# Optimization experiments

Hardware: AMD Instinct MI355X
Metric: run time of the kernel (lower is better)

Reference implementation:

```python
import jax, jax.numpy as jnp
import numpy as np

B = 4194304  # batch
H = 32       # hidden width of TinyMLP


def _xavier(key, fan_in, fan_out, gain=0.5):
    lim = gain * np.sqrt(6.0 / (fan_in + fan_out))
    return jax.random.uniform(key, (fan_in, fan_out), jnp.float32, -lim, lim)


def setup_inputs() -> dict:
    key = jax.random.key(0)
    ks = jax.random.split(key, 7)
    return {
        "x1": jax.random.normal(ks[0], (B,), jnp.float32),
        "x2": jax.random.normal(ks[1], (B,), jnp.float32),
        "y1": jax.random.normal(ks[2], (B,), jnp.float32),
        "y2": jax.random.normal(ks[3], (B,), jnp.float32),
        "W1": _xavier(ks[4], 2, H),
        "b1": jnp.zeros((H,), jnp.float32),
        "W2": _xavier(ks[5], H, H),
        "b2": jnp.zeros((H,), jnp.float32),
        "W3": _xavier(ks[6], H, 1),
        "b3": jnp.zeros((1,), jnp.float32),
    }


def reference(x1, x2, y1, y2, W1, b1, W2, b2, W3, b3):
    # Y: [B, 2]
    Y = jnp.stack([y1, y2], axis=1)

    def F_sum(Yv):
        h1 = jax.nn.sigmoid(Yv @ W1 + b1)   # [B, H]
        h2 = jax.nn.sigmoid(h1 @ W2 + b2)   # [B, H]
        return jnp.sum(h2 @ W3 + b3)        # scalar sum of F values

    dF_dY = jax.grad(F_sum)(Y)              # [B, 2], analytic input-gradient

    x1_out = x1 + dF_dY[:, 0]
    x2_out = x2 + dF_dY[:, 1]
    # Stack the 4 output streams as columns: (x1', x2', y1, y2)
    return jnp.stack([x1_out, x2_out, y1, y2], axis=1)
```

## Files before the change

### kernel.cpp

```cpp
#include <hip/hip_runtime.h>


#define H 32

typedef __attribute__((ext_vector_type(8))) short bf16x8;
typedef __attribute__((ext_vector_type(4))) float f32x4;
typedef __attribute__((ext_vector_type(2))) float f32x2;
typedef __attribute__((ext_vector_type(2))) __bf16 bfx2;

__device__ __forceinline__ int cvt_pk_bf16(float a, float b) {
    f32x2 f; f[0] = a; f[1] = b;
    bfx2 r = __builtin_convertvector(f, bfx2);
    return __builtin_bit_cast(int, r);
}

__device__ __forceinline__ unsigned short f2bf_trunc(float f) {
    unsigned u = __builtin_bit_cast(unsigned, f);
    return (unsigned short)((u + 0x8000u) >> 16);
}

#define NLOG2E (-1.4426950408889634f)

__global__ __launch_bounds__(256) void tinymlp_mfma_kernel(
    const float* __restrict__ x1, const float* __restrict__ x2,
    const float* __restrict__ y1, const float* __restrict__ y2,
    const float* __restrict__ W1, const float* __restrict__ b1,
    const float* __restrict__ W2, const float* __restrict__ b2,
    const float* __restrict__ W3,
    float4* __restrict__ out, int ntiles)
{
    __shared__ unsigned short lds_dz2[4][512];
    __shared__ float          lds_dh1[4][512];

    const int tid  = threadIdx.x;
    const int w    = tid >> 6;
    const int lane = tid & 63;
    const int m    = lane & 15;
    const int q    = lane >> 4;
    const int kb   = q * 8;

    bf16x8 bW2s_0, bW2s_1, bW2T_0, bW2T_1, bW1r;
    float w1a[8], w1b[8], b1v[8];
    #pragma unroll
    for (int j = 0; j < 8; ++j) {
        bW2s_0[j] = (short)f2bf_trunc(NLOG2E * W2[(kb + j) * H + m]);
        bW2s_1[j] = (short)f2bf_trunc(NLOG2E * W2[(kb + j) * H + m + 16]);
        bW2T_0[j] = (short)f2bf_trunc(W2[m * H + kb + j]);
        bW2T_1[j] = (short)f2bf_trunc(W2[(m + 16) * H + kb + j]);
        bW1r[j]   = (short)f2bf_trunc(W1[(m & 1) * H + kb + j]);
        w1a[j] = NLOG2E * W1[kb + j];
        w1b[j] = NLOG2E * W1[H + kb + j];
        b1v[j] = NLOG2E * b1[kb + j];
    }
    const float b2s0 = NLOG2E * b2[m];
    const float b2s1 = NLOG2E * b2[m + 16];
    f32x2 w3v; w3v[0] = W3[m]; w3v[1] = W3[m + 16];

    const int gwave  = (blockIdx.x * blockDim.x + tid) >> 6;
    const int nwaves = (gridDim.x * blockDim.x) >> 6;

    const int c    = m & 3;
    const int srow = q * 4 + c;
    const long start = (long)gwave * 16;
    const long step  = (long)nwaves * 16;
    const float* py1 = y1 + start + m;
    const float* py2 = y2 + start + m;
    const float* px1 = x1 + start + srow;
    const float* px2 = x2 + start + srow;
    const float* qy1 = y1 + start + srow;
    const float* qy2 = y2 + start + srow;
    float4*      po  = out + start + srow;

    unsigned short* dzp = &lds_dz2[w][(m >> 3) * 128 + (m & 7) + q * 32];

    for (int tile = gwave; tile < ntiles; tile += nwaves) {
        const float y1v = *py1;
        const float y2v = *py2;
        float xv1 = 0.f, xv2 = 0.f, yv3 = 0.f, yv4 = 0.f;
        if (m < 4) { xv1 = *px1; xv2 = *px2; yv3 = *qy1; yv4 = *qy2; }

        f32x2 h1dp[4];
        union { int i[4]; bf16x8 v; } uaH;
        #pragma unroll
        for (int t = 0; t < 4; ++t) {
            const int j = 2 * t;
            float z0 = fmaf(y1v, w1a[j],     fmaf(y2v, w1b[j],     b1v[j]));
            float z1 = fmaf(y1v, w1a[j + 1], fmaf(y2v, w1b[j + 1], b1v[j + 1]));
            float e0 = __builtin_amdgcn_exp2f(z0);
            float e1 = __builtin_amdgcn_exp2f(z1);
            float s0 = __builtin_amdgcn_rcpf(1.0f + e0);
            float s1 = __builtin_amdgcn_rcpf(1.0f + e1);
            f32x2 sv; sv[0] = s0; sv[1] = s1;
            h1dp[t] = __builtin_elementwise_fma(-sv, sv, sv);
            uaH.i[t] = cvt_pk_bf16(s0, s1);
        }

        f32x4 accZ0 = {b2s0, b2s0, b2s0, b2s0};
        f32x4 accZ1 = {b2s1, b2s1, b2s1, b2s1};
        accZ0 = __builtin_amdgcn_mfma_f32_16x16x32_bf16(uaH.v, bW2s_0, accZ0, 0, 0, 0);
        accZ1 = __builtin_amdgcn_mfma_f32_16x16x32_bf16(uaH.v, bW2s_1, accZ1, 0, 0, 0);

        #pragma unroll
        for (int r = 0; r < 4; ++r) {
            float e0 = __builtin_amdgcn_exp2f(accZ0[r]);
            float e1 = __builtin_amdgcn_exp2f(accZ1[r]);
            float s0 = __builtin_amdgcn_rcpf(1.0f + e0);
            float s1 = __builtin_amdgcn_rcpf(1.0f + e1);
            f32x2 sv; sv[0] = s0; sv[1] = s1;
            f32x2 dv = __builtin_elementwise_fma(-sv, sv, sv) * w3v;
            unsigned pk = (unsigned)cvt_pk_bf16(dv[0], dv[1]);
            dzp[r * 8]       = (unsigned short)pk;
            dzp[r * 8 + 256] = (unsigned short)(pk >> 16);
        }
        __builtin_amdgcn_wave_barrier();

        const bf16x8 aD = *(const bf16x8*)&lds_dz2[w][lane * 8];
        f32x4 accD0 = {0.f, 0.f, 0.f, 0.f}, accD1 = {0.f, 0.f, 0.f, 0.f};
        accD0 = __builtin_amdgcn_mfma_f32_16x16x32_bf16(aD, bW2T_0, accD0, 0, 0, 0);
        accD1 = __builtin_amdgcn_mfma_f32_16x16x32_bf16(aD, bW2T_1, accD1, 0, 0, 0);

        #pragma unroll
        for (int r = 0; r < 4; ++r) {
            const int row = q * 4 + r;
            lds_dh1[w][row * 32 + (((m >> 3) ^ r) << 3) + (m & 7)]       = accD0[r];
            lds_dh1[w][row * 32 + ((((m >> 3) | 2) ^ r) << 3) + (m & 7)] = accD1[r];
        }
        __builtin_amdgcn_wave_barrier();
        const float* pr = &lds_dh1[w][m * 32 + ((q ^ (m & 3)) << 3)];
        const f32x4 dlo = *(const f32x4*)pr;
        const f32x4 dhi = *(const f32x4*)(pr + 4);

        f32x2 p0, p1, p2, p3;
        p0[0] = dlo[0]; p0[1] = dlo[1]; p0 *= h1dp[0];
        p1[0] = dlo[2]; p1[1] = dlo[3]; p1 *= h1dp[1];
        p2[0] = dhi[0]; p2[1] = dhi[1]; p2 *= h1dp[2];
        p3[0] = dhi[2]; p3[1] = dhi[3]; p3 *= h1dp[3];
        union { int i[4]; bf16x8 v; } uaG;
        uaG.i[0] = cvt_pk_bf16(p0[0], p0[1]);
        uaG.i[1] = cvt_pk_bf16(p1[0], p1[1]);
        uaG.i[2] = cvt_pk_bf16(p2[0], p2[1]);
        uaG.i[3] = cvt_pk_bf16(p3[0], p3[1]);

        f32x4 accY = {0.f, 0.f, 0.f, 0.f};
        accY = __builtin_amdgcn_mfma_f32_16x16x32_bf16(uaG.v, bW1r, accY, 0, 0, 0);

        const float t0  = (c & 2) ? accY[2] : accY[0];
        const float t1  = (c & 2) ? accY[3] : accY[1];
        const float own = (c & 1) ? t1 : t0;
        const float vs  = (c & 1) ? t0 : t1;
        const float rcv = __shfl_xor(vs, 1);
        const float g1 = (m & 1) ? rcv : own;
        const float g2 = (m & 1) ? own : rcv;
        if (m < 4) {
            float4 o;
            o.x = xv1 + g1;
            o.y = xv2 + g2;
            o.z = yv3;
            o.w = yv4;
            *po = o;
        }
        __builtin_amdgcn_wave_barrier();

        py1 += step; py2 += step; px1 += step; px2 += step;
        qy1 += step; qy2 += step; po += step;
    }
}

extern "C" void kernel_launch(void* const* d_in, const int* in_sizes, int n_in,
                              void* d_out, int out_size, void* d_ws, size_t ws_size,
                              hipStream_t stream) {
    const float* x1 = (const float*)d_in[0];
    const float* x2 = (const float*)d_in[1];
    const float* y1 = (const float*)d_in[2];
    const float* y2 = (const float*)d_in[3];
    const float* W1 = (const float*)d_in[4];
    const float* b1 = (const float*)d_in[5];
    const float* W2 = (const float*)d_in[6];
    const float* b2 = (const float*)d_in[7];
    const float* W3 = (const float*)d_in[8];

    const int n = in_sizes[0];
    const int ntiles = n / 16;
    const int block = 256;
    const int grid = 2048;
    tinymlp_mfma_kernel<<<grid, block, 0, stream>>>(
        x1, x2, y1, y2, W1, b1, W2, b2, W3, (float4*)d_out, ntiles);
}
```

Before: 215.2 us.

## Transpose MFMA layout and move layer-1 onto MFMA with split-bf16 inputs

The kernel switches to a transposed MFMA formulation where the batch is the N dimension. The first layer now runs on MFMA using hi/lo bf16 splits of the inputs and weights plus a bias column. W3 is folded into the transposed W2 weights, and four reciprocals are batched into one rcp plus multiplies. A single LDS buffer with packed int2 stores replaces the old scalar scatter and float transposes, and launch bounds request 8 blocks per CU. The aim is to cut VALU transcendental and FMA work and LDS traffic per tile. The costs are an extra MFMA stage and extra LDS round-trips, and the batched reciprocal can overflow or lose precision when the product of the four terms gets large.

After: 212.5 us. No clear change (-1.2%).

```diff
diff --git a/kernel.cpp b/kernel.cpp
--- a/kernel.cpp
+++ b/kernel.cpp
@@ -2,26 +2,42 @@
 
 
 #define H 32
+#define NLOG2E (-1.4426950408889634f)
 
 typedef __attribute__((ext_vector_type(8))) short bf16x8;
 typedef __attribute__((ext_vector_type(4))) float f32x4;
 typedef __attribute__((ext_vector_type(2))) float f32x2;
 typedef __attribute__((ext_vector_type(2))) __bf16 bfx2;
 
+#define MFMA16 __builtin_amdgcn_mfma_f32_16x16x32_bf16
+
 __device__ __forceinline__ int cvt_pk_bf16(float a, float b) {
     f32x2 f; f[0] = a; f[1] = b;
     bfx2 r = __builtin_convertvector(f, bfx2);
     return __builtin_bit_cast(int, r);
 }
-
-__device__ __forceinline__ unsigned short f2bf_trunc(float f) {
-    unsigned u = __builtin_bit_cast(unsigned, f);
-    return (unsigned short)((u + 0x8000u) >> 16);
-}
-
-#define NLOG2E (-1.4426950408889634f)
-
-__global__ __launch_bounds__(256) void tinymlp_mfma_kernel(
+__device__ __forceinline__ unsigned f2bf(float f) {
+    return (unsigned)cvt_pk_bf16(f, 0.f) & 0xFFFFu;
+}
+__device__ __forceinline__ float bf2f(unsigned s) {
+    unsigned u = s << 16; return __builtin_bit_cast(float, u);
+}
+__device__ __forceinline__ float pklo(int p) {
+    unsigned u = (unsigned)p << 16; return __builtin_bit_cast(float, u);
+}
+__device__ __forceinline__ float pkhi(int p) {
+    unsigned u = (unsigned)p & 0xFFFF0000u; return __builtin_bit_cast(float, u);
+}
+
+__device__ __forceinline__ f32x4 rcp4(const f32x4 a) {
+    float m01 = a[0] * a[1], m23 = a[2] * a[3];
+    float r   = __builtin_amdgcn_rcpf(m01 * m23);
+    float r01 = r * m23, r23 = r * m01;
+    f32x4 s; s[0] = a[1] * r01; s[1] = a[0] * r01; s[2] = a[3] * r23; s[3] = a[2] * r23;
+    return s;
+}
+
+__global__ __launch_bounds__(256, 8) void tinymlp_mfma_kernel(
     const float* __restrict__ x1, const float* __restrict__ x2,
     const float* __restrict__ y1, const float* __restrict__ y2,
     const float* __restrict__ W1, const float* __restrict__ b1,
@@ -29,8 +45,7 @@
     const float* __restrict__ W3,
     float4* __restrict__ out, int ntiles)
 {
-    __shared__ unsigned short lds_dz2[4][512];
-    __shared__ float          lds_dh1[4][512];
+    __shared__ unsigned short lds0[4096];
 
     const int tid  = threadIdx.x;
     const int w    = tid >> 6;
@@ -39,130 +54,158 @@
     const int q    = lane >> 4;
     const int kb   = q * 8;
 
-    bf16x8 bW2s_0, bW2s_1, bW2T_0, bW2T_1, bW1r;
-    float w1a[8], w1b[8], b1v[8];
+    bf16x8 bW2s_0, bW2s_1, bW2T3_0, bW2T3_1, bW1r;
     #pragma unroll
     for (int j = 0; j < 8; ++j) {
-        bW2s_0[j] = (short)f2bf_trunc(NLOG2E * W2[(kb + j) * H + m]);
-        bW2s_1[j] = (short)f2bf_trunc(NLOG2E * W2[(kb + j) * H + m + 16]);
-        bW2T_0[j] = (short)f2bf_trunc(W2[m * H + kb + j]);
-        bW2T_1[j] = (short)f2bf_trunc(W2[(m + 16) * H + kb + j]);
-        bW1r[j]   = (short)f2bf_trunc(W1[(m & 1) * H + kb + j]);
-        w1a[j] = NLOG2E * W1[kb + j];
-        w1b[j] = NLOG2E * W1[H + kb + j];
-        b1v[j] = NLOG2E * b1[kb + j];
-    }
-    const float b2s0 = NLOG2E * b2[m];
-    const float b2s1 = NLOG2E * b2[m + 16];
-    f32x2 w3v; w3v[0] = W3[m]; w3v[1] = W3[m + 16];
+        bW2s_0[j] = (short)f2bf(NLOG2E * W2[(kb + j) * H + m]);
+        bW2s_1[j] = (short)f2bf(NLOG2E * W2[(kb + j) * H + m + 16]);
+        const float w3 = W3[kb + j];
+        bW2T3_0[j] = (short)f2bf(W2[m * H + kb + j] * w3);
+        bW2T3_1[j] = (short)f2bf(W2[(m + 16) * H + kb + j] * w3);
+        bW1r[j] = (m < 2) ? (short)f2bf(W1[m * H + kb + j]) : (short)0;
+    }
+
+    union { int i[4]; bf16x8 v; } uW1lo, uW1hi;
+    uW1lo.i[0] = uW1lo.i[1] = uW1lo.i[2] = uW1lo.i[3] = 0;
+    uW1hi.i[0] = uW1hi.i[1] = uW1hi.i[2] = uW1hi.i[3] = 0;
+    if (q == 0) {
+        #pragma unroll
+        for (int half = 0; half < 2; ++half) {
+            const int h = m + 16 * half;
+            const float wa = NLOG2E * W1[h];
+            const float wb = NLOG2E * W1[H + h];
+            const float bv = NLOG2E * b1[h];
+            const unsigned ah = f2bf(wa), bh = f2bf(wb);
+            const unsigned al = f2bf(wa - bf2f(ah)), bl = f2bf(wb - bf2f(bh));
+            const unsigned ch = f2bf(bv);
+            const unsigned cl = f2bf(bv - bf2f(ch));
+            int i0 = (int)(ah | (bh << 16));
+            int i1 = (int)(al | (bl << 16));
+            int i3 = (int)(ch | (cl << 16));
+            if (half == 0) { uW1lo.i[0] = i0; uW1lo.i[1] = i1; uW1lo.i[2] = i0; uW1lo.i[3] = i3; }
+            else           { uW1hi.i[0] = i0; uW1hi.i[1] = i1; uW1hi.i[2] = i0; uW1hi.i[3] = i3; }
+        }
+    }
+
+    f32x4 b2C0, b2C1;
+    {
+        const float4 t0 = ((const float4*)b2)[q];
+        const float4 t1 = ((const float4*)b2)[q + 4];
+        b2C0[0] = NLOG2E * t0.x; b2C0[1] = NLOG2E * t0.y; b2C0[2] = NLOG2E * t0.z; b2C0[3] = NLOG2E * t0.w;
+        b2C1[0] = NLOG2E * t1.x; b2C1[1] = NLOG2E * t1.y; b2C1[2] = NLOG2E * t1.z; b2C1[3] = NLOG2E * t1.w;
+    }
+
+    unsigned short*       wp = &lds0[w * 1024 + (q >> 1) * 128 + m * 8 + (q & 1) * 4];
+    const unsigned short* rp = &lds0[w * 1024 + lane * 8];
 
     const int gwave  = (blockIdx.x * blockDim.x + tid) >> 6;
     const int nwaves = (gridDim.x * blockDim.x) >> 6;
-
-    const int c    = m & 3;
-    const int srow = q * 4 + c;
-    const long start = (long)gwave * 16;
-    const long step  = (long)nwaves * 16;
-    const float* py1 = y1 + start + m;
-    const float* py2 = y2 + start + m;
-    const float* px1 = x1 + start + srow;
-    const float* px2 = x2 + start + srow;
-    const float* qy1 = y1 + start + srow;
-    const float* qy2 = y2 + start + srow;
-    float4*      po  = out + start + srow;
-
-    unsigned short* dzp = &lds_dz2[w][(m >> 3) * 128 + (m & 7) + q * 32];
+    unsigned idx = (unsigned)gwave * 16 + (unsigned)m;
+    const unsigned step = (unsigned)nwaves * 16;
 
     for (int tile = gwave; tile < ntiles; tile += nwaves) {
-        const float y1v = *py1;
-        const float y2v = *py2;
-        float xv1 = 0.f, xv2 = 0.f, yv3 = 0.f, yv4 = 0.f;
-        if (m < 4) { xv1 = *px1; xv2 = *px2; yv3 = *qy1; yv4 = *qy2; }
-
-        f32x2 h1dp[4];
-        union { int i[4]; bf16x8 v; } uaH;
-        #pragma unroll
-        for (int t = 0; t < 4; ++t) {
-            const int j = 2 * t;
-            float z0 = fmaf(y1v, w1a[j],     fmaf(y2v, w1b[j],     b1v[j]));
-            float z1 = fmaf(y1v, w1a[j + 1], fmaf(y2v, w1b[j + 1], b1v[j + 1]));
-            float e0 = __builtin_amdgcn_exp2f(z0);
-            float e1 = __builtin_amdgcn_exp2f(z1);
-            float s0 = __builtin_amdgcn_rcpf(1.0f + e0);
-            float s1 = __builtin_amdgcn_rcpf(1.0f + e1);
-            f32x2 sv; sv[0] = s0; sv[1] = s1;
-            h1dp[t] = __builtin_elementwise_fma(-sv, sv, sv);
-            uaH.i[t] = cvt_pk_bf16(s0, s1);
-        }
-
-        f32x4 accZ0 = {b2s0, b2s0, b2s0, b2s0};
-        f32x4 accZ1 = {b2s1, b2s1, b2s1, b2s1};
-        accZ0 = __builtin_amdgcn_mfma_f32_16x16x32_bf16(uaH.v, bW2s_0, accZ0, 0, 0, 0);
-        accZ1 = __builtin_amdgcn_mfma_f32_16x16x32_bf16(uaH.v, bW2s_1, accZ1, 0, 0, 0);
-
+        const float y1v = y1[idx];
+        const float y2v = y2[idx];
+        float xv1 = 0.f, xv2 = 0.f;
+        if (lane < 16) { xv1 = x1[idx]; xv2 = x2[idx]; }
+
+        const int pkHI = cvt_pk_bf16(y1v, y2v);
+        const float l1 = y1v - pklo(pkHI);
+        const float l2 = y2v - pkhi(pkHI);
+        const int pkLO = cvt_pk_bf16(l1, l2);
+        union { int i[4]; bf16x8 v; } uY;
+        uY.i[0] = pkHI; uY.i[1] = pkHI; uY.i[2] = pkLO; uY.i[3] = 0x3F803F80;
+
+        const f32x4 zf = {0.f, 0.f, 0.f, 0.f};
+
+        f32x4 zL = MFMA16(uW1lo.v, uY.v, zf, 0, 0, 0);
+        f32x4 zH = MFMA16(uW1hi.v, uY.v, zf, 0, 0, 0);
+
+        f32x4 aL, aH;
         #pragma unroll
         for (int r = 0; r < 4; ++r) {
-            float e0 = __builtin_amdgcn_exp2f(accZ0[r]);
-            float e1 = __builtin_amdgcn_exp2f(accZ1[r]);
-            float s0 = __builtin_amdgcn_rcpf(1.0f + e0);
-            float s1 = __builtin_amdgcn_rcpf(1.0f + e1);
-            f32x2 sv; sv[0] = s0; sv[1] = s1;
-            f32x2 dv = __builtin_elementwise_fma(-sv, sv, sv) * w3v;
-            unsigned pk = (unsigned)cvt_pk_bf16(dv[0], dv[1]);
-            dzp[r * 8]       = (unsigned short)pk;
-            dzp[r * 8 + 256] = (unsigned short)(pk >> 16);
-        }
-        __builtin_amdgcn_wave_barrier();
-
-        const bf16x8 aD = *(const bf16x8*)&lds_dz2[w][lane * 8];
-        f32x4 accD0 = {0.f, 0.f, 0.f, 0.f}, accD1 = {0.f, 0.f, 0.f, 0.f};
-        accD0 = __builtin_amdgcn_mfma_f32_16x16x32_bf16(aD, bW2T_0, accD0, 0, 0, 0);
-        accD1 = __builtin_amdgcn_mfma_f32_16x16x32_bf16(aD, bW2T_1, accD1, 0, 0, 0);
-
+            aL[r] = __builtin_amdgcn_exp2f(zL[r]);
+            aH[r] = __builtin_amdgcn_exp2f(zH[r]);
+        }
+        aL += 1.0f; aH += 1.0f;
+        const f32x4 sL = rcp4(aL);
+        const f32x4 sH = rcp4(aH);
+        const int P0 = cvt_pk_bf16(sL[0], sL[1]);
+        const int P1 = cvt_pk_bf16(sL[2], sL[3]);
+        const int P2 = cvt_pk_bf16(sH[0], sH[1]);
+        const int P3 = cvt_pk_bf16(sH[2], sH[3]);
+
+        int2 wv0; wv0.x = P0; wv0.y = P1;
+        int2 wv1; wv1.x = P2; wv1.y = P3;
+        *(int2*)wp         = wv0;
+        *(int2*)(wp + 256) = wv1;
+        __builtin_amdgcn_wave_barrier();
+        const bf16x8 uaH = *(const bf16x8*)rp;
+
+        f32x4 zzL = MFMA16(bW2s_0, uaH, b2C0, 0, 0, 0);
+        f32x4 zzH = MFMA16(bW2s_1, uaH, b2C1, 0, 0, 0);
+
+        f32x4 cL, cH;
         #pragma unroll
         for (int r = 0; r < 4; ++r) {
-            const int row = q * 4 + r;
-            lds_dh1[w][row * 32 + (((m >> 3) ^ r) << 3) + (m & 7)]       = accD0[r];
-            lds_dh1[w][row * 32 + ((((m >> 3) | 2) ^ r) << 3) + (m & 7)] = accD1[r];
-        }
-        __builtin_amdgcn_wave_barrier();
-        const float* pr = &lds_dh1[w][m * 32 + ((q ^ (m & 3)) << 3)];
-        const f32x4 dlo = *(const f32x4*)pr;
-        const f32x4 dhi = *(const f32x4*)(pr + 4);
-
-        f32x2 p0, p1, p2, p3;
-        p0[0] = dlo[0]; p0[1] = dlo[1]; p0 *= h1dp[0];
-        p1[0] = dlo[2]; p1[1] = dlo[3]; p1 *= h1dp[1];
-        p2[0] = dhi[0]; p2[1] = dhi[1]; p2 *= h1dp[2];
-        p3[0] = dhi[2]; p3[1] = dhi[3]; p3 *= h1dp[3];
-        union { int i[4]; bf16x8 v; } uaG;
-        uaG.i[0] = cvt_pk_bf16(p0[0], p0[1]);
-        uaG.i[1] = cvt_pk_bf16(p1[0], p1[1]);
-        uaG.i[2] = cvt_pk_bf16(p2[0], p2[1]);
-        uaG.i[3] = cvt_pk_bf16(p3[0], p3[1]);
-
-        f32x4 accY = {0.f, 0.f, 0.f, 0.f};
-        accY = __builtin_amdgcn_mfma_f32_16x16x32_bf16(uaG.v, bW1r, accY, 0, 0, 0);
-
-        const float t0  = (c & 2) ? accY[2] : accY[0];
-        const float t1  = (c & 2) ? accY[3] : accY[1];
-        const float own = (c & 1) ? t1 : t0;
-        const float vs  = (c & 1) ? t0 : t1;
-        const float rcv = __shfl_xor(vs, 1);
-        const float g1 = (m & 1) ? rcv : own;
-        const float g2 = (m & 1) ? own : rcv;
-        if (m < 4) {
+            cL[r] = __builtin_amdgcn_exp2f(zzL[r]);
+            cH[r] = __builtin_amdgcn_exp2f(zzH[r]);
+        }
+        cL += 1.0f; cH += 1.0f;
+        const f32x4 s2L = rcp4(cL);
+        const f32x4 s2H = rcp4(cH);
+        f32x2 d0; d0[0] = s2L[0]; d0[1] = s2L[1]; d0 = __builtin_elementwise_fma(-d0, d0, d0);
+        f32x2 d1; d1[0] = s2L[2]; d1[1] = s2L[3]; d1 = __builtin_elementwise_fma(-d1, d1, d1);
+        f32x2 d2; d2[0] = s2H[0]; d2[1] = s2H[1]; d2 = __builtin_elementwise_fma(-d2, d2, d2);
+        f32x2 d3; d3[0] = s2H[2]; d3[1] = s2H[3]; d3 = __builtin_elementwise_fma(-d3, d3, d3);
+
+        int2 qv0; qv0.x = cvt_pk_bf16(d0[0], d0[1]); qv0.y = cvt_pk_bf16(d1[0], d1[1]);
+        int2 qv1; qv1.x = cvt_pk_bf16(d2[0], d2[1]); qv1.y = cvt_pk_bf16(d3[0], d3[1]);
+        *(int2*)(wp + 512) = qv0;
+        *(int2*)(wp + 768) = qv1;
+        __builtin_amdgcn_wave_barrier();
+        const bf16x8 aD = *(const bf16x8*)(rp + 512);
+
+        f32x4 dLo = MFMA16(bW2T3_0, aD, zf, 0, 0, 0);
+        f32x4 dHi = MFMA16(bW2T3_1, aD, zf, 0, 0, 0);
+
+        f32x2 sv, gg;
+        sv[0] = pklo(P0); sv[1] = pkhi(P0);
+        f32x2 h0 = __builtin_elementwise_fma(-sv, sv, sv);
+        gg[0] = dLo[0]; gg[1] = dLo[1]; gg *= h0;
+        const int G0 = cvt_pk_bf16(gg[0], gg[1]);
+        sv[0] = pklo(P1); sv[1] = pkhi(P1);
+        h0 = __builtin_elementwise_fma(-sv, sv, sv);
+        gg[0] = dLo[2]; gg[1] = dLo[3]; gg *= h0;
+        const int G1 = cvt_pk_bf16(gg[0], gg[1]);
+        sv[0] = pklo(P2); sv[1] = pkhi(P2);
+        h0 = __builtin_elementwise_fma(-sv, sv, sv);
+        gg[0] = dHi[0]; gg[1] = dHi[1]; gg *= h0;
+        const int G2 = cvt_pk_bf16(gg[0], gg[1]);
+        sv[0] = pklo(P3); sv[1] = pkhi(P3);
+        h0 = __builtin_elementwise_fma(-sv, sv, sv);
+        gg[0] = dHi[2]; gg[1] = dHi[3]; gg *= h0;
+        const int G3 = cvt_pk_bf16(gg[0], gg[1]);
+
+        int2 gv0; gv0.x = G0; gv0.y = G1;
+        int2 gv1; gv1.x = G2; gv1.y = G3;
+        *(int2*)wp         = gv0;
+        *(int2*)(wp + 256) = gv1;
+        __builtin_amdgcn_wave_barrier();
+        const bf16x8 uaG = *(const bf16x8*)rp;
+
+        f32x4 accY = MFMA16(bW1r, uaG, zf, 0, 0, 0);
+
+        if (lane < 16) {
             float4 o;
-            o.x = xv1 + g1;
-            o.y = xv2 + g2;
-            o.z = yv3;
-            o.w = yv4;
-            *po = o;
-        }
-        __builtin_amdgcn_wave_barrier();
-
-        py1 += step; py2 += step; px1 += step; px2 += step;
-        qy1 += step; qy2 += step; po += step;
+            o.x = xv1 + accY[0];
+            o.y = xv2 + accY[1];
+            o.z = y1v;
+            o.w = y2v;
+            out[idx] = o;
+        }
+        __builtin_amdgcn_wave_barrier();
+        idx += step;
     }
 }
 
```
